# Optimization experiments

Hardware: AMD Instinct MI355X
Metric: run time of the kernel (lower is better)

Reference implementation:

```python
import jax, jax.numpy as jnp
import numpy as np

GROUPS = 32
HEADS = 4
EPS_GN = 1e-5
EPS_DEN = 1e-6


def group_norm(x, gamma, beta):
    b, c, h, w = x.shape
    xg = x.reshape(b, GROUPS, (c // GROUPS) * h * w)
    mu = xg.mean(axis=-1, keepdims=True)
    var = xg.var(axis=-1, keepdims=True)
    xn = ((xg - mu) * jax.lax.rsqrt(var + EPS_GN)).reshape(b, c, h, w)
    return xn * gamma[None, :, None, None] + beta[None, :, None, None]


def setup_inputs() -> dict:
    key = jax.random.key(0)
    ks = jax.random.split(key, 4)
    b, c, h, w = 16, 256, 64, 64
    x = jax.random.normal(ks[0], (b, c, h, w), dtype=jnp.float32)
    gamma = jnp.ones((c,), jnp.float32)
    beta = jnp.zeros((c,), jnp.float32)
    w_qkv = jax.random.normal(ks[1], (3 * c, c), jnp.float32) * (1.0 / np.sqrt(c))
    b_qkv = jnp.zeros((3 * c,), jnp.float32)
    w_out = jax.random.normal(ks[2], (c, c), jnp.float32) * (1.0 / np.sqrt(c))
    b_out = jnp.zeros((c,), jnp.float32)
    return {"x": x, "gamma": gamma, "beta": beta, "w_qkv": w_qkv,
            "b_qkv": b_qkv, "w_out": w_out, "b_out": b_out}


def reference(x, gamma, beta, w_qkv, b_qkv, w_out, b_out):
    b, c, h, w = x.shape
    d = c // HEADS
    n = h * w
    xn = group_norm(x, gamma, beta)
    # 1x1 conv == channel GEMM: [b,3c,h,w]
    qkv = jnp.einsum('bchw,oc->bohw', xn, w_qkv) + b_qkv[None, :, None, None]
    q, k, v = jnp.split(qkv, 3, axis=1)
    # b (heads d) h w -> b heads d n
    q = q.reshape(b, HEADS, d, n)
    k = k.reshape(b, HEADS, d, n)
    v = v.reshape(b, HEADS, d, n)
    q = jax.nn.elu(q) + 1.0
    k = jax.nn.elu(k) + 1.0
    k_sum = k.sum(axis=-1)                                 # [b,H,d]
    kv = jnp.einsum('bhdn,bhen->bhde', k, v)               # [b,H,d,d]
    out = jnp.einsum('bhde,bhdn->bhen', kv, q)             # [b,H,d,n]
    denom = jnp.einsum('bhdn,bhd->bhn', q, k_sum)          # [b,H,n]
    out = out / (denom[:, :, None, :] + EPS_DEN)
    out = out.reshape(b, c, h, w)
    out = jnp.einsum('bchw,oc->bohw', out, w_out) + b_out[None, :, None, None]
    return out + x
```

## Files before the change

kernel.cpp:

```cpp
#include <hip/hip_runtime.h>
#include <stdint.h>

#define BATCH 16
#define CH    256
#define NSP   4096
#define NH    4
#define HD    64

typedef __attribute__((ext_vector_type(8))) short bf16x8;
typedef __attribute__((ext_vector_type(4))) float f32x4;
typedef __attribute__((ext_vector_type(4))) unsigned int u32x4;

__device__ __forceinline__ short f2bf(float f) {
    union { float f; unsigned u; } v; v.f = f;
    unsigned r = (v.u + 0x7fffu + ((v.u >> 16) & 1u)) >> 16;
    return (short)r;
}
__device__ __forceinline__ float bf2f(short s) {
    union { float f; unsigned u; } v; v.u = ((unsigned)(unsigned short)s) << 16;
    return v.f;
}

__global__ __launch_bounds__(256) void k_pre(
        const float* __restrict__ x, const float* __restrict__ wq, const float* __restrict__ wo,
        float* __restrict__ mu, float* __restrict__ rstd,
        short* __restrict__ wq_bf, short* __restrict__ wo_bf) {
    int bg = blockIdx.x;
    if (bg < 512) {
        const float4* p = (const float4*)(x + (size_t)bg * 32768);
        float s = 0.f, sq = 0.f;
        for (int i = threadIdx.x; i < 8192; i += 256) {
            float4 v = p[i];
            s  += v.x + v.y + v.z + v.w;
            sq += v.x * v.x + v.y * v.y + v.z * v.z + v.w * v.w;
        }
        for (int off = 32; off; off >>= 1) { s += __shfl_down(s, off); sq += __shfl_down(sq, off); }
        __shared__ float ls[4], lq[4];
        int w = threadIdx.x >> 6;
        if ((threadIdx.x & 63) == 0) { ls[w] = s; lq[w] = sq; }
        __syncthreads();
        if (threadIdx.x == 0) {
            float S = ls[0] + ls[1] + ls[2] + ls[3];
            float Q = lq[0] + lq[1] + lq[2] + lq[3];
            float m = S / 32768.f;
            float var = Q / 32768.f - m * m;
            mu[bg] = m; rstd[bg] = rsqrtf(var + 1e-5f);
        }
    } else {
        int idx = ((bg - 512) * 256 + threadIdx.x) * 4;
        float4 v;
        short* dst;
        if (idx < 196608) { v = *(const float4*)(wq + idx); dst = wq_bf + idx; }
        else              { v = *(const float4*)(wo + (idx - 196608)); dst = wo_bf + (idx - 196608); }
        unsigned p0 = ((unsigned)(unsigned short)f2bf(v.x)) | (((unsigned)(unsigned short)f2bf(v.y)) << 16);
        unsigned p1 = ((unsigned)(unsigned short)f2bf(v.z)) | (((unsigned)(unsigned short)f2bf(v.w)) << 16);
        uint2 pk; pk.x = p0; pk.y = p1;
        *(uint2*)dst = pk;
    }
}

__global__ __launch_bounds__(256) void k_gnqkv(
        const float* __restrict__ x, const float* __restrict__ gamma, const float* __restrict__ beta,
        const float* __restrict__ mu, const float* __restrict__ rstd,
        const short* __restrict__ wq_bf, const float* __restrict__ b_qkv,
        short* __restrict__ q_t, short* __restrict__ kvp_bf, float* __restrict__ ksp) {
    int b = blockIdx.y, nt = blockIdx.x;
    int n0 = nt * 64;
    __shared__ short Blds[64 * 264];
    __shared__ union UR {
        struct { short kst[64 * 72]; short vst[64 * 72]; } s;
        short cst[64 * 136];
    } R;
    int t = threadIdx.x, lane = t & 63, wv = t >> 6, lr = lane & 15, quad = lane >> 4;

    {
        const float* xb = x + (size_t)b * CH * NSP;
        int m = t & 15, cq = t >> 4;
        #pragma unroll 4
        for (int cb = 0; cb < 16; cb++) {
            int c = cb * 16 + cq;
            int g = c >> 3;
            float sc = rstd[b * 32 + g] * gamma[c];
            float sh = beta[c] - mu[b * 32 + g] * sc;
            float4 v = *(const float4*)(xb + (size_t)c * NSP + n0 + m * 4);
            float vv[4] = {v.x, v.y, v.z, v.w};
            #pragma unroll
            for (int j = 0; j < 4; j++) {
                int n = m * 4 + j;
                int cc = c ^ (((n >> 4) & 3) << 3);
                Blds[n * 264 + cc] = f2bf(vv[j] * sc + sh);
            }
        }
    }
    __syncthreads();

    for (int h = 0; h < 4; h++) {
        int br0 = (wv < 2 ? 256 : 512) + h * 64;
        int sub = (wv & 1) * 32;
        const short* wr = wq_bf + (size_t)(br0 + sub + lr) * 256 + quad * 8;
        bf16x8 A0[8], A1[8];
        #pragma unroll
        for (int kk = 0; kk < 8; kk++) {
            A0[kk] = *(const bf16x8*)(wr + kk * 32);
            A1[kk] = *(const bf16x8*)(wr + 16 * 256 + kk * 32);
        }
        f32x4 acc[2][4] = {};
        #pragma unroll
        for (int kk = 0; kk < 8; kk++) {
            bf16x8 bfr[4];
            #pragma unroll
            for (int ni = 0; ni < 4; ni++) {
                int rr = ni * 16 + lr;
                bfr[ni] = *(const bf16x8*)(Blds + rr * 264 + ((kk * 32 + quad * 8) ^ (((rr >> 4) & 3) << 3)));
            }
            #pragma unroll
            for (int ni = 0; ni < 4; ni++) {
                acc[0][ni] = __builtin_amdgcn_mfma_f32_16x16x32_bf16(A0[kk], bfr[ni], acc[0][ni], 0, 0, 0);
                acc[1][ni] = __builtin_amdgcn_mfma_f32_16x16x32_bf16(A1[kk], bfr[ni], acc[1][ni], 0, 0, 0);
            }
        }
        __syncthreads();
        short* dst = (wv < 2) ? R.s.kst : R.s.vst;
        bool is_k = (wv < 2);
        #pragma unroll
        for (int mi = 0; mi < 2; mi++)
          #pragma unroll
          for (int ni = 0; ni < 4; ni++)
            #pragma unroll
            for (int r = 0; r < 4; r++) {
                int ol = sub + mi * 16 + quad * 4 + r;
                int nl = ni * 16 + lr;
                float v = acc[mi][ni][r] + b_qkv[br0 + ol];
                if (is_k) v = v > 0.f ? v + 1.f : __expf(v);
                dst[ol * 72 + nl] = f2bf(v);
            }
        __syncthreads();
        {
            int d = t >> 2, nq = (t & 3) * 16;
            float s = 0.f;
            #pragma unroll
            for (int j = 0; j < 16; j++) s += bf2f(R.s.kst[d * 72 + nq + j]);
            s += __shfl_down(s, 2);
            s += __shfl_down(s, 1);
            if ((t & 3) == 0) ksp[((size_t)(b * 4 + h) * 64 + nt) * 64 + d] = s;
        }
        f32x4 acc2[4] = {};
        #pragma unroll
        for (int kk = 0; kk < 64; kk += 32) {
            bf16x8 af = *(const bf16x8*)(R.s.vst + (wv * 16 + lr) * 72 + kk + quad * 8);
            bf16x8 bfk[4];
            #pragma unroll
            for (int ni = 0; ni < 4; ni++)
                bfk[ni] = *(const bf16x8*)(R.s.kst + (ni * 16 + lr) * 72 + kk + quad * 8);
            #pragma unroll
            for (int ni = 0; ni < 4; ni++)
                acc2[ni] = __builtin_amdgcn_mfma_f32_16x16x32_bf16(af, bfk[ni], acc2[ni], 0, 0, 0);
        }
        short* kvdst = kvp_bf + ((size_t)(b * 4 + h) * 64 + nt) * 4096;
        #pragma unroll
        for (int ni = 0; ni < 4; ni++)
            #pragma unroll
            for (int r = 0; r < 4; r++)
                kvdst[(wv * 16 + quad * 4 + r) * 64 + ni * 16 + lr] = f2bf(acc2[ni][r]);
    }

    for (int mtq = 0; mtq < 2; mtq++) {
        int wm = wv * 32;
        const short* wr = wq_bf + (size_t)(mtq * 128 + wm + lr) * 256 + quad * 8;
        bf16x8 A0[8], A1[8];
        #pragma unroll
        for (int kk = 0; kk < 8; kk++) {
            A0[kk] = *(const bf16x8*)(wr + kk * 32);
            A1[kk] = *(const bf16x8*)(wr + 16 * 256 + kk * 32);
        }
        f32x4 acc[2][4] = {};
        #pragma unroll
        for (int kk = 0; kk < 8; kk++) {
            bf16x8 bfr[4];
            #pragma unroll
            for (int ni = 0; ni < 4; ni++) {
                int rr = ni * 16 + lr;
                bfr[ni] = *(const bf16x8*)(Blds + rr * 264 + ((kk * 32 + quad * 8) ^ (((rr >> 4) & 3) << 3)));
            }
            #pragma unroll
            for (int ni = 0; ni < 4; ni++) {
                acc[0][ni] = __builtin_amdgcn_mfma_f32_16x16x32_bf16(A0[kk], bfr[ni], acc[0][ni], 0, 0, 0);
                acc[1][ni] = __builtin_amdgcn_mfma_f32_16x16x32_bf16(A1[kk], bfr[ni], acc[1][ni], 0, 0, 0);
            }
        }
        __syncthreads();
        #pragma unroll
        for (int mi = 0; mi < 2; mi++)
          #pragma unroll
          for (int ni = 0; ni < 4; ni++)
            #pragma unroll
            for (int r = 0; r < 4; r++) {
                int ol = wm + mi * 16 + quad * 4 + r;
                int nl = ni * 16 + lr;
                float v = acc[mi][ni][r] + b_qkv[mtq * 128 + ol];
                v = v > 0.f ? v + 1.f : __expf(v);
                R.cst[nl * 136 + ol] = f2bf(v);
            }
        __syncthreads();
        #pragma unroll
        for (int i = 0; i < 4; i++) {
            int ch = t + i * 256;
            int row = ch >> 4, o8 = (ch & 15) * 8;
            int hh = mtq * 2 + (o8 >> 6), d0 = o8 & 63;
            *(u32x4*)(q_t + ((size_t)(b * 4 + hh) * NSP + n0 + row) * HD + d0) =
                *(const u32x4*)(R.cst + row * 136 + o8);
        }
    }
}

__global__ __launch_bounds__(256) void k_kv_reduce(
        const short* __restrict__ kvp_bf, const float* __restrict__ ksp,
        short* __restrict__ kvT_bf, float* __restrict__ ksum_g) {
    int p = blockIdx.x, bh = blockIdx.y;
    int t = threadIdx.x, lane = t & 63, grp = t >> 6;
    int chunk = p * 64 + lane;
    const short* base = kvp_bf + (size_t)bh * 64 * 4096 + chunk * 8;
    float s[8] = {};
    for (int ntc = grp * 16; ntc < grp * 16 + 16; ntc++) {
        bf16x8 v = *(const bf16x8*)(base + (size_t)ntc * 4096);
        #pragma unroll
        for (int j = 0; j < 8; j++) s[j] += bf2f(v[j]);
    }
    __shared__ float red[4][64][8];
    if (grp) {
        #pragma unroll
        for (int j = 0; j < 8; j++) red[grp][lane][j] = s[j];
    }
    __syncthreads();
    if (grp == 0) {
        bf16x8 rv;
        #pragma unroll
        for (int j = 0; j < 8; j++) {
            float v = s[j] + red[1][lane][j] + red[2][lane][j] + red[3][lane][j];
            rv[j] = f2bf(v);
        }
        *(bf16x8*)(kvT_bf + (size_t)bh * 4096 + chunk * 8) = rv;
    }
    if (p == 0) {
        const float* kb = ksp + (size_t)bh * 64 * 64 + lane;
        float ss = 0.f;
        for (int ntc = grp * 16; ntc < grp * 16 + 16; ntc++) ss += kb[(size_t)ntc * 64];
        __syncthreads();
        red[grp][lane][0] = ss;
        __syncthreads();
        if (grp == 0) ksum_g[bh * 64 + lane] = ss + red[1][lane][0] + red[2][lane][0] + red[3][lane][0];
    }
}

__global__ __launch_bounds__(256) void k_attn_out(
        const short* __restrict__ q_t, const short* __restrict__ kvT_bf,
        const float* __restrict__ ksum_g, const short* __restrict__ wo_bf,
        const float* __restrict__ b_out, const float* __restrict__ x,
        float* __restrict__ out) {
    int b = blockIdx.y, nt = blockIdx.x;
    int n0 = nt * 64;
    __shared__ short Battn[64 * 264];
    __shared__ short ql[64 * 72];
    __shared__ short kvl[64 * 72];
    __shared__ float dnp[4][64];
    int t = threadIdx.x, lane = t & 63, wv = t >> 6, lr = lane & 15, quad = lane >> 4;

    for (int h = 0; h < 4; h++) {
        int bh = b * 4 + h;
        #pragma unroll
        for (int i = 0; i < 2; i++) {
            int ch = t + i * 256;
            int row = ch >> 3, dc = (ch & 7) * 8;
            *(u32x4*)(ql + row * 72 + dc) =
                *(const u32x4*)(q_t + ((size_t)bh * NSP + n0 + row) * HD + dc);
            *(u32x4*)(kvl + row * 72 + dc) =
                *(const u32x4*)(kvT_bf + (size_t)bh * 4096 + row * 64 + dc);
        }
        __syncthreads();
        {
            int n = t & 63, q0 = wv * 16;
            const float* ks = ksum_g + bh * 64 + q0;
            float s = 0.f;
            #pragma unroll
            for (int j = 0; j < 16; j += 8) {
                bf16x8 qv = *(const bf16x8*)(ql + n * 72 + q0 + j);
                #pragma unroll
                for (int u = 0; u < 8; u++) s += bf2f(qv[u]) * ks[j + u];
            }
            dnp[wv][n] = s;
        }
        f32x4 acc[4] = {};
        #pragma unroll
        for (int kk = 0; kk < 64; kk += 32) {
            bf16x8 af = *(const bf16x8*)(ql + (wv * 16 + lr) * 72 + kk + quad * 8);
            bf16x8 bfr[4];
            #pragma unroll
            for (int ni = 0; ni < 4; ni++)
                bfr[ni] = *(const bf16x8*)(kvl + (ni * 16 + lr) * 72 + kk + quad * 8);
            #pragma unroll
            for (int ni = 0; ni < 4; ni++)
                acc[ni] = __builtin_amdgcn_mfma_f32_16x16x32_bf16(af, bfr[ni], acc[ni], 0, 0, 0);
        }
        __syncthreads();
        float dn[4];
        #pragma unroll
        for (int r = 0; r < 4; r++) {
            int n = wv * 16 + quad * 4 + r;
            dn[r] = 1.f / (dnp[0][n] + dnp[1][n] + dnp[2][n] + dnp[3][n] + 1e-6f);
        }
        #pragma unroll
        for (int ni = 0; ni < 4; ni++)
            #pragma unroll
            for (int r = 0; r < 4; r++) {
                int n = wv * 16 + quad * 4 + r;
                Battn[n * 264 + h * 64 + ni * 16 + lr] = f2bf(acc[ni][r] * dn[r]);
            }
        __syncthreads();
    }

    for (int p = 0; p < 2; p++) {
        int rbase = p * 128 + wv * 32;
        const short* wr = wo_bf + (size_t)(rbase + lr) * 256 + quad * 8;
        bf16x8 A0[8], A1[8];
        #pragma unroll
        for (int kk = 0; kk < 8; kk++) {
            A0[kk] = *(const bf16x8*)(wr + kk * 32);
            A1[kk] = *(const bf16x8*)(wr + 16 * 256 + kk * 32);
        }
        f32x4 acc[2][4] = {};
        #pragma unroll
        for (int kk = 0; kk < 8; kk++) {
            bf16x8 bfr[4];
            #pragma unroll
            for (int ni = 0; ni < 4; ni++)
                bfr[ni] = *(const bf16x8*)(Battn + (ni * 16 + lr) * 264 + kk * 32 + quad * 8);
            #pragma unroll
            for (int ni = 0; ni < 4; ni++) {
                acc[0][ni] = __builtin_amdgcn_mfma_f32_16x16x32_bf16(A0[kk], bfr[ni], acc[0][ni], 0, 0, 0);
                acc[1][ni] = __builtin_amdgcn_mfma_f32_16x16x32_bf16(A1[kk], bfr[ni], acc[1][ni], 0, 0, 0);
            }
        }
        #pragma unroll
        for (int mi = 0; mi < 2; mi++)
          #pragma unroll
          for (int ni = 0; ni < 4; ni++)
            #pragma unroll
            for (int r = 0; r < 4; r++) {
                int o = rbase + mi * 16 + quad * 4 + r;
                int nl = ni * 16 + lr;
                size_t idx = ((size_t)b * CH + o) * NSP + n0 + nl;
                out[idx] = acc[mi][ni][r] + b_out[o] + x[idx];
            }
    }
}

extern "C" void kernel_launch(void* const* d_in, const int* in_sizes, int n_in,
                              void* d_out, int out_size, void* d_ws, size_t ws_size,
                              hipStream_t stream) {
    const float* x     = (const float*)d_in[0];
    const float* gamma = (const float*)d_in[1];
    const float* beta  = (const float*)d_in[2];
    const float* w_qkv = (const float*)d_in[3];
    const float* b_qkv = (const float*)d_in[4];
    const float* w_out = (const float*)d_in[5];
    const float* b_out = (const float*)d_in[6];
    float* out = (float*)d_out;

    char* ws = (char*)d_ws;
    size_t off = 0;
    float* mu     = (float*)(ws + off); off += 2048;
    float* rstd   = (float*)(ws + off); off += 2048;
    short* wq_bf  = (short*)(ws + off); off += (size_t)768 * 256 * 2;
    short* wo_bf  = (short*)(ws + off); off += (size_t)256 * 256 * 2;
    short* q_t    = (short*)(ws + off); off += (size_t)BATCH * NSP * CH * 2;
    short* kvp_bf = (short*)(ws + off); off += (size_t)64 * 64 * 4096 * 2;
    float* ksp    = (float*)(ws + off); off += (size_t)64 * 64 * 64 * 4;
    short* kvT_bf = (short*)(ws + off); off += (size_t)64 * 4096 * 2;
    float* ksum_g = (float*)(ws + off); off += (size_t)64 * 64 * 4;

    if (ws_size < off) return;

    k_pre<<<768, 256, 0, stream>>>(x, w_qkv, w_out, mu, rstd, wq_bf, wo_bf);
    k_gnqkv<<<dim3(64, 16), 256, 0, stream>>>(x, gamma, beta, mu, rstd, wq_bf, b_qkv, q_t, kvp_bf, ksp);
    k_kv_reduce<<<dim3(8, 64), 256, 0, stream>>>(kvp_bf, ksp, kvT_bf, ksum_g);
    k_attn_out<<<dim3(64, 16), 256, 0, stream>>>(q_t, kvT_bf, ksum_g, wo_bf, b_out, x, out);
}
```

Before: 278.5 us.

## Precompute GroupNorm scale/shift tables, batch x loads, tune occupancy and scheduling

k_pre now writes per-(batch,channel) scale and shift tables, so k_gnqkv no longer recomputes them from mu/rstd/gamma/beta. The GroupNorm staging loop issues all 16 float4 loads of x before converting, which raises memory-level parallelism at the cost of more registers. Launch bounds of 3 blocks per CU are added to k_gnqkv and k_attn_out, the outer head and pass loops are kept rolled, and sched_barriers are placed after the weight fragment loads to steer register allocation and instruction scheduling. Capping registers to reach that occupancy could cause spills.

```diff
diff --git a/kernel.cpp b/kernel.cpp
--- a/kernel.cpp
+++ b/kernel.cpp
@@ -23,12 +23,14 @@
 
 __global__ __launch_bounds__(256) void k_pre(
         const float* __restrict__ x, const float* __restrict__ wq, const float* __restrict__ wo,
-        float* __restrict__ mu, float* __restrict__ rstd,
+        const float* __restrict__ gamma, const float* __restrict__ beta,
+        float* __restrict__ sc_tab, float* __restrict__ sh_tab,
         short* __restrict__ wq_bf, short* __restrict__ wo_bf) {
     int bg = blockIdx.x;
     if (bg < 512) {
         const float4* p = (const float4*)(x + (size_t)bg * 32768);
         float s = 0.f, sq = 0.f;
+        #pragma unroll 4
         for (int i = threadIdx.x; i < 8192; i += 256) {
             float4 v = p[i];
             s  += v.x + v.y + v.z + v.w;
@@ -44,7 +46,15 @@
             float Q = lq[0] + lq[1] + lq[2] + lq[3];
             float m = S / 32768.f;
             float var = Q / 32768.f - m * m;
-            mu[bg] = m; rstd[bg] = rsqrtf(var + 1e-5f);
+            ls[0] = m; lq[0] = rsqrtf(var + 1e-5f);
+        }
+        __syncthreads();
+        if (threadIdx.x < 8) {
+            int b = bg >> 5, g = bg & 31, c = g * 8 + threadIdx.x;
+            float r = lq[0], mm = ls[0];
+            float sc = r * gamma[c];
+            sc_tab[b * 256 + c] = sc;
+            sh_tab[b * 256 + c] = beta[c] - mm * sc;
         }
     } else {
         int idx = ((bg - 512) * 256 + threadIdx.x) * 4;
@@ -59,9 +69,9 @@
     }
 }
 
-__global__ __launch_bounds__(256) void k_gnqkv(
-        const float* __restrict__ x, const float* __restrict__ gamma, const float* __restrict__ beta,
-        const float* __restrict__ mu, const float* __restrict__ rstd,
+__global__ __launch_bounds__(256, 3) void k_gnqkv(
+        const float* __restrict__ x,
+        const float* __restrict__ sc_tab, const float* __restrict__ sh_tab,
         const short* __restrict__ wq_bf, const float* __restrict__ b_qkv,
         short* __restrict__ q_t, short* __restrict__ kvp_bf, float* __restrict__ ksp) {
     int b = blockIdx.y, nt = blockIdx.x;
@@ -74,36 +84,43 @@
     int t = threadIdx.x, lane = t & 63, wv = t >> 6, lr = lane & 15, quad = lane >> 4;
 
     {
-        const float* xb = x + (size_t)b * CH * NSP;
+        const float* xb = x + (size_t)b * CH * NSP + n0;
+        const float* scb = sc_tab + b * 256;
+        const float* shb = sh_tab + b * 256;
         int m = t & 15, cq = t >> 4;
-        #pragma unroll 4
+        float4 vv[16];
+        float scA[16], shA[16];
+        #pragma unroll
         for (int cb = 0; cb < 16; cb++) {
             int c = cb * 16 + cq;
-            int g = c >> 3;
-            float sc = rstd[b * 32 + g] * gamma[c];
-            float sh = beta[c] - mu[b * 32 + g] * sc;
-            float4 v = *(const float4*)(xb + (size_t)c * NSP + n0 + m * 4);
-            float vv[4] = {v.x, v.y, v.z, v.w};
+            vv[cb] = *(const float4*)(xb + (size_t)c * NSP + m * 4);
+            scA[cb] = scb[c]; shA[cb] = shb[c];
+        }
+        #pragma unroll
+        for (int cb = 0; cb < 16; cb++) {
+            int c = cb * 16 + cq;
+            float va[4] = {vv[cb].x, vv[cb].y, vv[cb].z, vv[cb].w};
             #pragma unroll
             for (int j = 0; j < 4; j++) {
                 int n = m * 4 + j;
                 int cc = c ^ (((n >> 4) & 3) << 3);
-                Blds[n * 264 + cc] = f2bf(vv[j] * sc + sh);
+                Blds[n * 264 + cc] = f2bf(va[j] * scA[cb] + shA[cb]);
             }
         }
     }
     __syncthreads();
 
+    #pragma unroll 1
     for (int h = 0; h < 4; h++) {
         int br0 = (wv < 2 ? 256 : 512) + h * 64;
         int sub = (wv & 1) * 32;
-        const short* wr = wq_bf + (size_t)(br0 + sub + lr) * 256 + quad * 8;
         bf16x8 A0[8], A1[8];
         #pragma unroll
         for (int kk = 0; kk < 8; kk++) {
-            A0[kk] = *(const bf16x8*)(wr + kk * 32);
-            A1[kk] = *(const bf16x8*)(wr + 16 * 256 + kk * 32);
-        }
+            A0[kk] = *(const bf16x8*)(wq_bf + (size_t)(br0 + sub + lr) * 256 + kk * 32 + quad * 8);
+            A1[kk] = *(const bf16x8*)(wq_bf + (size_t)(br0 + sub + 16 + lr) * 256 + kk * 32 + quad * 8);
+        }
+        __builtin_amdgcn_sched_barrier(0);
         f32x4 acc[2][4] = {};
         #pragma unroll
         for (int kk = 0; kk < 8; kk++) {
@@ -164,15 +181,16 @@
                 kvdst[(wv * 16 + quad * 4 + r) * 64 + ni * 16 + lr] = f2bf(acc2[ni][r]);
     }
 
+    #pragma unroll 1
     for (int mtq = 0; mtq < 2; mtq++) {
         int wm = wv * 32;
-        const short* wr = wq_bf + (size_t)(mtq * 128 + wm + lr) * 256 + quad * 8;
         bf16x8 A0[8], A1[8];
         #pragma unroll
         for (int kk = 0; kk < 8; kk++) {
-            A0[kk] = *(const bf16x8*)(wr + kk * 32);
-            A1[kk] = *(const bf16x8*)(wr + 16 * 256 + kk * 32);
-        }
+            A0[kk] = *(const bf16x8*)(wq_bf + (size_t)(mtq * 128 + wm + lr) * 256 + kk * 32 + quad * 8);
+            A1[kk] = *(const bf16x8*)(wq_bf + (size_t)(mtq * 128 + wm + 16 + lr) * 256 + kk * 32 + quad * 8);
+        }
+        __builtin_amdgcn_sched_barrier(0);
         f32x4 acc[2][4] = {};
         #pragma unroll
         for (int kk = 0; kk < 8; kk++) {
@@ -252,7 +270,7 @@
     }
 }
 
-__global__ __launch_bounds__(256) void k_attn_out(
+__global__ __launch_bounds__(256, 3) void k_attn_out(
         const short* __restrict__ q_t, const short* __restrict__ kvT_bf,
         const float* __restrict__ ksum_g, const short* __restrict__ wo_bf,
         const float* __restrict__ b_out, const float* __restrict__ x,
@@ -265,6 +283,7 @@
     __shared__ float dnp[4][64];
     int t = threadIdx.x, lane = t & 63, wv = t >> 6, lr = lane & 15, quad = lane >> 4;
 
+    #pragma unroll 1
     for (int h = 0; h < 4; h++) {
         int bh = b * 4 + h;
         #pragma unroll
@@ -318,15 +337,16 @@
         __syncthreads();
     }
 
+    #pragma unroll 1
     for (int p = 0; p < 2; p++) {
         int rbase = p * 128 + wv * 32;
-        const short* wr = wo_bf + (size_t)(rbase + lr) * 256 + quad * 8;
         bf16x8 A0[8], A1[8];
         #pragma unroll
         for (int kk = 0; kk < 8; kk++) {
-            A0[kk] = *(const bf16x8*)(wr + kk * 32);
-            A1[kk] = *(const bf16x8*)(wr + 16 * 256 + kk * 32);
-        }
+            A0[kk] = *(const bf16x8*)(wo_bf + (size_t)(rbase + lr) * 256 + kk * 32 + quad * 8);
+            A1[kk] = *(const bf16x8*)(wo_bf + (size_t)(rbase + 16 + lr) * 256 + kk * 32 + quad * 8);
+        }
+        __builtin_amdgcn_sched_barrier(0);
         f32x4 acc[2][4] = {};
         #pragma unroll
         for (int kk = 0; kk < 8; kk++) {
@@ -368,8 +388,8 @@
 
     char* ws = (char*)d_ws;
     size_t off = 0;
-    float* mu     = (float*)(ws + off); off += 2048;
-    float* rstd   = (float*)(ws + off); off += 2048;
+    float* sc_tab = (float*)(ws + off); off += (size_t)16 * 256 * 4;
+    float* sh_tab = (float*)(ws + off); off += (size_t)16 * 256 * 4;
     short* wq_bf  = (short*)(ws + off); off += (size_t)768 * 256 * 2;
     short* wo_bf  = (short*)(ws + off); off += (size_t)256 * 256 * 2;
     short* q_t    = (short*)(ws + off); off += (size_t)BATCH * NSP * CH * 2;
@@ -380,8 +400,8 @@
 
     if (ws_size < off) return;
 
-    k_pre<<<768, 256, 0, stream>>>(x, w_qkv, w_out, mu, rstd, wq_bf, wo_bf);
-    k_gnqkv<<<dim3(64, 16), 256, 0, stream>>>(x, gamma, beta, mu, rstd, wq_bf, b_qkv, q_t, kvp_bf, ksp);
-    k_kv_reduce<<<dim3(8, 64), 256, 0, stream>>>(kvp_bf, ksp, kvT_bf, ksum_g);
+    k_pre<<<768, 256, 0, stream>>>(x, w_qkv, w_out, gamma, beta, sc_tab, sh_tab, wq_bf, wo_bf);
+    k_gnqkv<<<dim3(64, 16), 256, 0, stream>>>(x, sc_tab, sh_tab, wq_bf, b_qkv, q_t, kvp_bf, ksp);
+    k_kv_reduce<<<dim3(2 * 4, 64), 256, 0, stream>>>(kvp_bf, ksp, kvT_bf, ksum_g);
     k_attn_out<<<dim3(64, 16), 256, 0, stream>>>(q_t, kvT_bf, ksum_g, wo_bf, b_out, x, out);
 }
```

Result: faster. 271.9 us (-2.3%).

## Fuse per-head attention into output projection and cut registers and LDS

Applied to the files above, without the earlier changes.

The attention-output kernel no longer stages all four heads into a 64x256 LDS buffer before the output projection. Each head's normalized result now goes into a small 64x64 tile and is immediately accumulated into a 64x64-per-wave output register tile, with smaller LDS padding and a launch bound asking for 4 blocks per SM. The QKV GEMMs stop preloading the whole 8-step A operand into registers and instead load the A fragments from global memory on each k-step. The float-to-bf16 conversion switches to the library intrinsic. The intent is to lower LDS and register use so more blocks fit per SM, at the cost of more global weight reads and a 64-row padding stride that may cause LDS bank conflicts.

```diff
diff --git a/kernel.cpp b/kernel.cpp
--- a/kernel.cpp
+++ b/kernel.cpp
@@ -1,4 +1,5 @@
 #include <hip/hip_runtime.h>
+#include <hip/hip_bf16.h>
 #include <stdint.h>
 
 #define BATCH 16
@@ -12,9 +13,9 @@
 typedef __attribute__((ext_vector_type(4))) unsigned int u32x4;
 
 __device__ __forceinline__ short f2bf(float f) {
-    union { float f; unsigned u; } v; v.f = f;
-    unsigned r = (v.u + 0x7fffu + ((v.u >> 16) & 1u)) >> 16;
-    return (short)r;
+    __hip_bfloat16 h = __float2bfloat16(f);
+    union { __hip_bfloat16 h; short s; } u; u.h = h;
+    return u.s;
 }
 __device__ __forceinline__ float bf2f(short s) {
     union { float f; unsigned u; } v; v.u = ((unsigned)(unsigned short)s) << 16;
@@ -76,7 +77,6 @@
     {
         const float* xb = x + (size_t)b * CH * NSP;
         int m = t & 15, cq = t >> 4;
-        #pragma unroll 4
         for (int cb = 0; cb < 16; cb++) {
             int c = cb * 16 + cq;
             int g = c >> 3;
@@ -95,29 +95,24 @@
     __syncthreads();
 
     for (int h = 0; h < 4; h++) {
-        int br0 = (wv < 2 ? 256 : 512) + h * 64;
+        int base_row = (wv < 2 ? 256 : 512) + h * 64;
         int sub = (wv & 1) * 32;
-        const short* wr = wq_bf + (size_t)(br0 + sub + lr) * 256 + quad * 8;
-        bf16x8 A0[8], A1[8];
-        #pragma unroll
-        for (int kk = 0; kk < 8; kk++) {
-            A0[kk] = *(const bf16x8*)(wr + kk * 32);
-            A1[kk] = *(const bf16x8*)(wr + 16 * 256 + kk * 32);
-        }
         f32x4 acc[2][4] = {};
-        #pragma unroll
-        for (int kk = 0; kk < 8; kk++) {
-            bf16x8 bfr[4];
+        for (int k0 = 0; k0 < 256; k0 += 32) {
+            bf16x8 afr[2], bfr[4];
+            #pragma unroll
+            for (int mi = 0; mi < 2; mi++)
+                afr[mi] = *(const bf16x8*)(wq_bf + (size_t)(base_row + sub + mi * 16 + lr) * 256 + k0 + quad * 8);
             #pragma unroll
             for (int ni = 0; ni < 4; ni++) {
                 int rr = ni * 16 + lr;
-                bfr[ni] = *(const bf16x8*)(Blds + rr * 264 + ((kk * 32 + quad * 8) ^ (((rr >> 4) & 3) << 3)));
-            }
-            #pragma unroll
-            for (int ni = 0; ni < 4; ni++) {
-                acc[0][ni] = __builtin_amdgcn_mfma_f32_16x16x32_bf16(A0[kk], bfr[ni], acc[0][ni], 0, 0, 0);
-                acc[1][ni] = __builtin_amdgcn_mfma_f32_16x16x32_bf16(A1[kk], bfr[ni], acc[1][ni], 0, 0, 0);
-            }
+                bfr[ni] = *(const bf16x8*)(Blds + rr * 264 + ((k0 + quad * 8) ^ (((rr >> 4) & 3) << 3)));
+            }
+            #pragma unroll
+            for (int mi = 0; mi < 2; mi++)
+                #pragma unroll
+                for (int ni = 0; ni < 4; ni++)
+                    acc[mi][ni] = __builtin_amdgcn_mfma_f32_16x16x32_bf16(afr[mi], bfr[ni], acc[mi][ni], 0, 0, 0);
         }
         __syncthreads();
         short* dst = (wv < 2) ? R.s.kst : R.s.vst;
@@ -130,7 +125,7 @@
             for (int r = 0; r < 4; r++) {
                 int ol = sub + mi * 16 + quad * 4 + r;
                 int nl = ni * 16 + lr;
-                float v = acc[mi][ni][r] + b_qkv[br0 + ol];
+                float v = acc[mi][ni][r] + b_qkv[base_row + ol];
                 if (is_k) v = v > 0.f ? v + 1.f : __expf(v);
                 dst[ol * 72 + nl] = f2bf(v);
             }
@@ -165,28 +160,23 @@
     }
 
     for (int mtq = 0; mtq < 2; mtq++) {
+        f32x4 acc[2][4] = {};
         int wm = wv * 32;
-        const short* wr = wq_bf + (size_t)(mtq * 128 + wm + lr) * 256 + quad * 8;
-        bf16x8 A0[8], A1[8];
-        #pragma unroll
-        for (int kk = 0; kk < 8; kk++) {
-            A0[kk] = *(const bf16x8*)(wr + kk * 32);
-            A1[kk] = *(const bf16x8*)(wr + 16 * 256 + kk * 32);
-        }
-        f32x4 acc[2][4] = {};
-        #pragma unroll
-        for (int kk = 0; kk < 8; kk++) {
-            bf16x8 bfr[4];
+        for (int k0 = 0; k0 < 256; k0 += 32) {
+            bf16x8 afr[2], bfr[4];
+            #pragma unroll
+            for (int mi = 0; mi < 2; mi++)
+                afr[mi] = *(const bf16x8*)(wq_bf + (size_t)(mtq * 128 + wm + mi * 16 + lr) * 256 + k0 + quad * 8);
             #pragma unroll
             for (int ni = 0; ni < 4; ni++) {
                 int rr = ni * 16 + lr;
-                bfr[ni] = *(const bf16x8*)(Blds + rr * 264 + ((kk * 32 + quad * 8) ^ (((rr >> 4) & 3) << 3)));
-            }
-            #pragma unroll
-            for (int ni = 0; ni < 4; ni++) {
-                acc[0][ni] = __builtin_amdgcn_mfma_f32_16x16x32_bf16(A0[kk], bfr[ni], acc[0][ni], 0, 0, 0);
-                acc[1][ni] = __builtin_amdgcn_mfma_f32_16x16x32_bf16(A1[kk], bfr[ni], acc[1][ni], 0, 0, 0);
-            }
+                bfr[ni] = *(const bf16x8*)(Blds + rr * 264 + ((k0 + quad * 8) ^ (((rr >> 4) & 3) << 3)));
+            }
+            #pragma unroll
+            for (int mi = 0; mi < 2; mi++)
+                #pragma unroll
+                for (int ni = 0; ni < 4; ni++)
+                    acc[mi][ni] = __builtin_amdgcn_mfma_f32_16x16x32_bf16(afr[mi], bfr[ni], acc[mi][ni], 0, 0, 0);
         }
         __syncthreads();
         #pragma unroll
@@ -252,28 +242,32 @@
     }
 }
 
-__global__ __launch_bounds__(256) void k_attn_out(
+__global__ __launch_bounds__(256, 4) void k_attn_out(
         const short* __restrict__ q_t, const short* __restrict__ kvT_bf,
         const float* __restrict__ ksum_g, const short* __restrict__ wo_bf,
         const float* __restrict__ b_out, const float* __restrict__ x,
         float* __restrict__ out) {
     int b = blockIdx.y, nt = blockIdx.x;
     int n0 = nt * 64;
-    __shared__ short Battn[64 * 264];
-    __shared__ short ql[64 * 72];
-    __shared__ short kvl[64 * 72];
+    __shared__ short ql[64 * 68];
+    __shared__ short kvl[64 * 68];
+    __shared__ short Bh[64 * 68];
     __shared__ float dnp[4][64];
     int t = threadIdx.x, lane = t & 63, wv = t >> 6, lr = lane & 15, quad = lane >> 4;
 
+    f32x4 aco[4][4] = {};
+    int r0 = wv * 64;
+
+    #pragma unroll 1
     for (int h = 0; h < 4; h++) {
         int bh = b * 4 + h;
         #pragma unroll
         for (int i = 0; i < 2; i++) {
             int ch = t + i * 256;
             int row = ch >> 3, dc = (ch & 7) * 8;
-            *(u32x4*)(ql + row * 72 + dc) =
+            *(u32x4*)(ql + row * 68 + dc) =
                 *(const u32x4*)(q_t + ((size_t)bh * NSP + n0 + row) * HD + dc);
-            *(u32x4*)(kvl + row * 72 + dc) =
+            *(u32x4*)(kvl + row * 68 + dc) =
                 *(const u32x4*)(kvT_bf + (size_t)bh * 4096 + row * 64 + dc);
         }
         __syncthreads();
@@ -283,75 +277,69 @@
             float s = 0.f;
             #pragma unroll
             for (int j = 0; j < 16; j += 8) {
-                bf16x8 qv = *(const bf16x8*)(ql + n * 72 + q0 + j);
+                bf16x8 qv = *(const bf16x8*)(ql + n * 68 + q0 + j);
                 #pragma unroll
                 for (int u = 0; u < 8; u++) s += bf2f(qv[u]) * ks[j + u];
             }
             dnp[wv][n] = s;
         }
-        f32x4 acc[4] = {};
+        f32x4 acc2[4] = {};
+        int nr = wv * 16;
         #pragma unroll
         for (int kk = 0; kk < 64; kk += 32) {
-            bf16x8 af = *(const bf16x8*)(ql + (wv * 16 + lr) * 72 + kk + quad * 8);
+            bf16x8 af = *(const bf16x8*)(ql + (nr + lr) * 68 + kk + quad * 8);
             bf16x8 bfr[4];
             #pragma unroll
             for (int ni = 0; ni < 4; ni++)
-                bfr[ni] = *(const bf16x8*)(kvl + (ni * 16 + lr) * 72 + kk + quad * 8);
+                bfr[ni] = *(const bf16x8*)(kvl + (ni * 16 + lr) * 68 + kk + quad * 8);
             #pragma unroll
             for (int ni = 0; ni < 4; ni++)
-                acc[ni] = __builtin_amdgcn_mfma_f32_16x16x32_bf16(af, bfr[ni], acc[ni], 0, 0, 0);
+                acc2[ni] = __builtin_amdgcn_mfma_f32_16x16x32_bf16(af, bfr[ni], acc2[ni], 0, 0, 0);
         }
         __syncthreads();
         float dn[4];
         #pragma unroll
         for (int r = 0; r < 4; r++) {
-            int n = wv * 16 + quad * 4 + r;
+            int n = nr + quad * 4 + r;
             dn[r] = 1.f / (dnp[0][n] + dnp[1][n] + dnp[2][n] + dnp[3][n] + 1e-6f);
         }
         #pragma unroll
         for (int ni = 0; ni < 4; ni++)
             #pragma unroll
             for (int r = 0; r < 4; r++) {
-                int n = wv * 16 + quad * 4 + r;
-                Battn[n * 264 + h * 64 + ni * 16 + lr] = f2bf(acc[ni][r] * dn[r]);
-            }
-        __syncthreads();
-    }
-
-    for (int p = 0; p < 2; p++) {
-        int rbase = p * 128 + wv * 32;
-        const short* wr = wo_bf + (size_t)(rbase + lr) * 256 + quad * 8;
-        bf16x8 A0[8], A1[8];
-        #pragma unroll
-        for (int kk = 0; kk < 8; kk++) {
-            A0[kk] = *(const bf16x8*)(wr + kk * 32);
-            A1[kk] = *(const bf16x8*)(wr + 16 * 256 + kk * 32);
-        }
-        f32x4 acc[2][4] = {};
-        #pragma unroll
-        for (int kk = 0; kk < 8; kk++) {
+                int n = nr + quad * 4 + r;
+                Bh[n * 68 + ni * 16 + lr] = f2bf(acc2[ni][r] * dn[r]);
+            }
+        __syncthreads();
+        #pragma unroll
+        for (int kk = 0; kk < 2; kk++) {
+            bf16x8 A[4];
+            #pragma unroll
+            for (int mi = 0; mi < 4; mi++)
+                A[mi] = *(const bf16x8*)(wo_bf + (size_t)(r0 + mi * 16 + lr) * 256 + h * 64 + kk * 32 + quad * 8);
             bf16x8 bfr[4];
             #pragma unroll
-            for (int ni = 0; ni < 4; ni++)
-                bfr[ni] = *(const bf16x8*)(Battn + (ni * 16 + lr) * 264 + kk * 32 + quad * 8);
-            #pragma unroll
-            for (int ni = 0; ni < 4; ni++) {
-                acc[0][ni] = __builtin_amdgcn_mfma_f32_16x16x32_bf16(A0[kk], bfr[ni], acc[0][ni], 0, 0, 0);
-                acc[1][ni] = __builtin_amdgcn_mfma_f32_16x16x32_bf16(A1[kk], bfr[ni], acc[1][ni], 0, 0, 0);
-            }
-        }
-        #pragma unroll
-        for (int mi = 0; mi < 2; mi++)
-          #pragma unroll
-          for (int ni = 0; ni < 4; ni++)
-            #pragma unroll
-            for (int r = 0; r < 4; r++) {
-                int o = rbase + mi * 16 + quad * 4 + r;
-                int nl = ni * 16 + lr;
-                size_t idx = ((size_t)b * CH + o) * NSP + n0 + nl;
-                out[idx] = acc[mi][ni][r] + b_out[o] + x[idx];
-            }
-    }
+            for (int nj = 0; nj < 4; nj++)
+                bfr[nj] = *(const bf16x8*)(Bh + (nj * 16 + lr) * 68 + kk * 32 + quad * 8);
+            #pragma unroll
+            for (int mi = 0; mi < 4; mi++)
+                #pragma unroll
+                for (int nj = 0; nj < 4; nj++)
+                    aco[mi][nj] = __builtin_amdgcn_mfma_f32_16x16x32_bf16(A[mi], bfr[nj], aco[mi][nj], 0, 0, 0);
+        }
+    }
+
+    #pragma unroll
+    for (int mi = 0; mi < 4; mi++)
+      #pragma unroll
+      for (int nj = 0; nj < 4; nj++)
+        #pragma unroll
+        for (int r = 0; r < 4; r++) {
+            int o = r0 + mi * 16 + quad * 4 + r;
+            int nl = nj * 16 + lr;
+            size_t idx = ((size_t)b * CH + o) * NSP + n0 + nl;
+            out[idx] = aco[mi][nj][r] + b_out[o] + x[idx];
+        }
 }
 
 extern "C" void kernel_launch(void* const* d_in, const int* in_sizes, int n_in,
```

New measurement: 259.3 us. 6.9% less time.
